# Kernel optimization log

Hardware: AMD Instinct MI355X
Metric: run time of the kernel (lower is better)

The kernel has to match this reference:

```python
import jax, jax.numpy as jnp
import numpy as np

SERIES_LEN = 4096
D_EMB = 1024
D_V = 1024
HURST = 0.7
H = HURST - 0.5          # exponent used by the module
DT = 1.0 / SERIES_LEN
EPS = 1e-8


def _attn_matrix():
    # Lower-triangular fractional power-law matrix A2[i, j]:
    #   j <  i : ((i - j) * dt + 1e-8) ** (hurst - 0.5)
    #   j == i : 1e-8 ** (hurst - 0.5)
    #   j >  i : 0
    i = jnp.arange(SERIES_LEN, dtype=jnp.int32)[:, None]
    j = jnp.arange(SERIES_LEN, dtype=jnp.int32)[None, :]
    diff = jnp.clip(i - j, 1, None).astype(jnp.float32)  # safe base for fractional power
    lower = jnp.where(i > j, (diff * DT + EPS) ** H, 0.0)
    diag = jnp.eye(SERIES_LEN, dtype=jnp.float32) * (EPS ** H)
    return lower + diag  # (L, L) float32


def setup_inputs() -> dict:
    key = jax.random.key(0)
    k1, k2 = jax.random.split(key)
    embed_series = jax.random.normal(k1, (D_EMB, SERIES_LEN), dtype=jnp.float32)
    # nn.Linear(d_emb, d_v, bias=False) weight has shape (d_v, d_emb)
    Wv_weight = jax.random.normal(k2, (D_V, D_EMB), dtype=jnp.float32) * (1.0 / np.sqrt(D_EMB))
    return {"embed_series": embed_series, "Wv_weight": Wv_weight}


def reference(embed_series, Wv_weight):
    # V (original, d_v x L) = Wv(embed_series.T).T ; output[i, c] = sum_j A2[i, j] * V[c, j]
    # => out = A2 @ (embed_series.T @ Wv_weight.T), shape (L, d_v)
    A2 = _attn_matrix()                                   # (L, L) lower triangular
    Y = jnp.einsum('el,ve->lv', embed_series, Wv_weight)  # (L, d_v)
    return A2 @ Y                                         # (L, d_v)
```

## Files before the change

kernel.cpp:

```cpp
#include <hip/hip_runtime.h>
#include <hip/hip_bf16.h>
#include <cstdint>
#include <cstddef>


#define L_SER 4096
#define DEMB  1024
#define DV    1024

#define R_STRIDE 4224
#define R_O0     4096

typedef __bf16 bf16_t;
typedef __attribute__((ext_vector_type(8))) __bf16 bf16x8;
typedef __attribute__((ext_vector_type(4))) float f32x4;

__device__ __forceinline__ void glds16(const bf16_t* g, bf16_t* l) {
    __builtin_amdgcn_global_load_lds(
        (const __attribute__((address_space(1))) unsigned int*)(const void*)g,
        (__attribute__((address_space(3))) unsigned int*)(void*)l,
        16, 0, 0);
}

__global__ void prep_kernel(const float* __restrict__ E, const float* __restrict__ W,
                            bf16_t* __restrict__ Eb, bf16_t* __restrict__ Wb,
                            bf16_t* __restrict__ R) {
    const int b = blockIdx.x;
    if (b < 132) {
        int idx = b * 256 + threadIdx.x;
        int s = idx / R_STRIDE;
        int x = idx - s * R_STRIDE;
        int d = R_O0 + s - x;
        float v = 0.0f;
        if (d >= 0 && d < L_SER)
            v = powf((d == 0) ? 1e-8f : ((float)d * (1.0f / (float)L_SER) + 1e-8f), 0.2f);
        R[idx] = (bf16_t)v;
    } else if (b < 132 + 2048) {
        int idx = (b - 132) * 256 + threadIdx.x;
        const f32x4* s = (const f32x4*)E;
        f32x4 v0 = s[idx * 2], v1 = s[idx * 2 + 1];
        bf16x8 o;
        o[0] = (bf16_t)v0[0]; o[1] = (bf16_t)v0[1]; o[2] = (bf16_t)v0[2]; o[3] = (bf16_t)v0[3];
        o[4] = (bf16_t)v1[0]; o[5] = (bf16_t)v1[1]; o[6] = (bf16_t)v1[2]; o[7] = (bf16_t)v1[3];
        ((bf16x8*)Eb)[idx] = o;
    } else {
        int idx = (b - 2180) * 256 + threadIdx.x;
        const f32x4* s = (const f32x4*)W;
        f32x4 v0 = s[idx * 2], v1 = s[idx * 2 + 1];
        bf16x8 o;
        o[0] = (bf16_t)v0[0]; o[1] = (bf16_t)v0[1]; o[2] = (bf16_t)v0[2]; o[3] = (bf16_t)v0[3];
        o[4] = (bf16_t)v1[0]; o[5] = (bf16_t)v1[1]; o[6] = (bf16_t)v1[2]; o[7] = (bf16_t)v1[3];
        ((bf16x8*)Wb)[idx] = o;
    }
}

#define GA_STAGE(SBOFS)                                                      \
    _Pragma("unroll")                                                        \
    for (int c = 0; c < 4; ++c) {                                            \
        glds16(pA[c], &sA[(SBOFS) + (c * 32 + wave * 8) * 64]);              \
        glds16(pB[c], &sB[(SBOFS) + (c * 32 + wave * 8) * 64]);              \
        pA[c] += 64; pB[c] += 64;                                            \
    }

#define GA_COMPUTE(SBOFS)                                                    \
    _Pragma("unroll")                                                        \
    for (int kk = 0; kk < 2; ++kk) {                                         \
        const int co = kk ? coff1 : coff0;                                   \
        bf16x8 afr[4], bfr[4];                                               \
        _Pragma("unroll")                                                    \
        for (int tm = 0; tm < 4; ++tm)                                       \
            afr[tm] = *(const bf16x8*)&sA[(SBOFS) + (wm * 64 + tm * 16 + ln) * 64 + co]; \
        _Pragma("unroll")                                                    \
        for (int tn = 0; tn < 4; ++tn)                                       \
            bfr[tn] = *(const bf16x8*)&sB[(SBOFS) + (wn * 64 + tn * 16 + ln) * 64 + co]; \
        _Pragma("unroll")                                                    \
        for (int tm = 0; tm < 4; ++tm)                                       \
            _Pragma("unroll")                                                \
            for (int tn = 0; tn < 4; ++tn)                                   \
                acc[tm][tn] = __builtin_amdgcn_mfma_f32_16x16x32_bf16(afr[tm], bfr[tn], acc[tm][tn], 0, 0, 0); \
    }

__global__ __launch_bounds__(256, 2) void gemm_a_kernel(const bf16_t* __restrict__ R,
                                                        const bf16_t* __restrict__ Eb,
                                                        bf16_t* __restrict__ T0,
                                                        bf16_t* __restrict__ T1) {
    __shared__ __align__(16) bf16_t sA[2 * 128 * 64];
    __shared__ __align__(16) bf16_t sB[2 * 128 * 64];

    const int bid = blockIdx.x;
    int I, nb, h;
    if (bid < 256) { I = bid >> 3;                nb = bid & 7;         h = 0; }
    else           { I = 31 - ((bid - 256) >> 3); nb = (bid - 256) & 7; h = 1; }
    const int i0 = I * 128;
    const int n0 = nb * 128;
    const int nsteps = I + 1;
    const int j0b = h ? 64 * (I + 1) : 0;
    bf16_t* __restrict__ Tout = h ? T1 : T0;

    const int tid  = threadIdx.x;
    const int wave = tid >> 6;
    const int lane = tid & 63;
    const int quad = lane >> 4;
    const int ln   = lane & 15;
    const int wm   = wave >> 1;
    const int wn   = wave & 1;

    const int lrow = lane >> 3;
    const int lch  = (lane & 7) ^ lrow;
    const int rsw   = ln & 7;
    const int coff0 = ((quad ^ rsw)) * 8;
    const int coff1 = (((4 + quad) ^ rsw)) * 8;

    f32x4 acc[4][4];
#pragma unroll
    for (int a = 0; a < 4; ++a)
#pragma unroll
        for (int b = 0; b < 4; ++b) acc[a][b] = (f32x4){0, 0, 0, 0};

    const bf16_t* pA[4];
    const bf16_t* pB[4];
#pragma unroll
    for (int c = 0; c < 4; ++c) {
        int r = c * 32 + wave * 8 + lrow;
        pA[c] = R + (size_t)(r & 7) * R_STRIDE + (R_O0 - i0 + j0b - 8 * (r >> 3) + lch * 8);
        pB[c] = Eb + (size_t)(n0 + r) * L_SER + j0b + lch * 8;
    }

    GA_STAGE(0)
    for (int s = 0;; s += 2) {
        __syncthreads();
        if (s + 1 < nsteps) { GA_STAGE(128 * 64) }
        GA_COMPUTE(0)
        if (s + 1 >= nsteps) break;
        __syncthreads();
        if (s + 2 < nsteps) { GA_STAGE(0) }
        GA_COMPUTE(128 * 64)
        if (s + 2 >= nsteps) break;
    }

#pragma unroll
    for (int tm = 0; tm < 4; ++tm) {
        int row_base = i0 + wm * 64 + tm * 16 + quad * 4;
#pragma unroll
        for (int tn = 0; tn < 4; ++tn) {
            int col = n0 + wn * 64 + tn * 16 + ln;
#pragma unroll
            for (int r = 0; r < 4; ++r)
                Tout[(size_t)(row_base + r) * DEMB + col] = (bf16_t)acc[tm][tn][r];
        }
    }
}

#define GB_STAGE_A(SBOFS, RA)                                                \
    _Pragma("unroll")                                                        \
    for (int c = 0; c < 2; ++c)                                              \
        *(bf16x8*)&sA[(SBOFS) + aofs[c]] = RA[c];

#define GB_LOAD_A(RA)                                                        \
    _Pragma("unroll")                                                        \
    for (int c = 0; c < 2; ++c) {                                            \
        bf16x8 t0 = *(const bf16x8*)p0[c];                                   \
        bf16x8 t1 = *(const bf16x8*)p1[c];                                   \
        bf16x8 o;                                                            \
        _Pragma("unroll")                                                    \
        for (int u = 0; u < 8; ++u) o[u] = (bf16_t)((float)t0[u] + (float)t1[u]); \
        RA[c] = o;                                                           \
        p0[c] += 64; p1[c] += 64;                                            \
    }

#define GB_STAGE_B(SBOFS)                                                    \
    _Pragma("unroll")                                                        \
    for (int c = 0; c < 4; ++c) {                                            \
        glds16(pW[c], &sB[(SBOFS) + (c * 32 + wave * 8) * 64]);              \
        pW[c] += 64;                                                         \
    }

#define GB_COMPUTE(SBOFS_A, SBOFS_B)                                         \
    _Pragma("unroll")                                                        \
    for (int kk = 0; kk < 2; ++kk) {                                         \
        const int co = kk ? coff1 : coff0;                                   \
        bf16x8 afr[2], bfr[4];                                               \
        _Pragma("unroll")                                                    \
        for (int tm = 0; tm < 2; ++tm)                                       \
            afr[tm] = *(const bf16x8*)&sA[(SBOFS_A) + (wm * 32 + tm * 16 + ln) * 64 + co]; \
        _Pragma("unroll")                                                    \
        for (int tn = 0; tn < 4; ++tn)                                       \
            bfr[tn] = *(const bf16x8*)&sB[(SBOFS_B) + (wn * 64 + tn * 16 + ln) * 64 + co]; \
        _Pragma("unroll")                                                    \
        for (int tm = 0; tm < 2; ++tm)                                       \
            _Pragma("unroll")                                                \
            for (int tn = 0; tn < 4; ++tn)                                   \
                acc[tm][tn] = __builtin_amdgcn_mfma_f32_16x16x32_bf16(afr[tm], bfr[tn], acc[tm][tn], 0, 0, 0); \
    }

__global__ __launch_bounds__(256, 2) void gemm_b_kernel(const bf16_t* __restrict__ T0,
                                                        const bf16_t* __restrict__ T1,
                                                        const bf16_t* __restrict__ Wb,
                                                        float* __restrict__ out) {
    __shared__ __align__(16) bf16_t sA[2 * 64 * 64];
    __shared__ __align__(16) bf16_t sB[2 * 128 * 64];

    const int bid = blockIdx.x;
    const int ib = bid >> 3;
    const int nb = bid & 7;
    const int i0 = ib * 64;
    const int n0 = nb * 128;

    const int tid  = threadIdx.x;
    const int wave = tid >> 6;
    const int lane = tid & 63;
    const int quad = lane >> 4;
    const int ln   = lane & 15;
    const int wm   = wave >> 1;
    const int wn   = wave & 1;
    const int srow = tid >> 3;
    const int t8   = tid & 7;

    const int lrow = lane >> 3;
    const int lch  = (lane & 7) ^ lrow;
    const int rsw   = ln & 7;
    const int coff0 = ((quad ^ rsw)) * 8;
    const int coff1 = (((4 + quad) ^ rsw)) * 8;

    int aofs[2];
#pragma unroll
    for (int c = 0; c < 2; ++c)
        aofs[c] = (c * 32 + srow) * 64 + (t8 ^ (srow & 7)) * 8;

    f32x4 acc[2][4];
#pragma unroll
    for (int a = 0; a < 2; ++a)
#pragma unroll
        for (int b = 0; b < 4; ++b) acc[a][b] = (f32x4){0, 0, 0, 0};

    const int nsteps = DEMB / 64;

    const bf16_t* p0[2];
    const bf16_t* p1[2];
    const bf16_t* pW[4];
    bf16x8 ra0[2], ra1[2];
#pragma unroll
    for (int c = 0; c < 2; ++c) {
        size_t arow = (size_t)(i0 + c * 32 + srow) * DEMB + t8 * 8;
        p0[c] = T0 + arow;
        p1[c] = T1 + arow;
    }
#pragma unroll
    for (int c = 0; c < 4; ++c)
        pW[c] = Wb + (size_t)(n0 + c * 32 + wave * 8 + lrow) * DEMB + lch * 8;

    GB_LOAD_A(ra0)
    GB_LOAD_A(ra1)
    GB_STAGE_B(0)

    for (int s = 0;; s += 2) {
        GB_STAGE_A(0, ra0)
        __syncthreads();
        if (s + 2 < nsteps) { GB_LOAD_A(ra0) }
        if (s + 1 < nsteps) { GB_STAGE_B(128 * 64) }
        GB_COMPUTE(0, 0)
        GB_STAGE_A(64 * 64, ra1)
        __syncthreads();
        if (s + 3 < nsteps) { GB_LOAD_A(ra1) }
        if (s + 2 < nsteps) { GB_STAGE_B(0) }
        GB_COMPUTE(64 * 64, 128 * 64)
        if (s + 2 >= nsteps) break;
    }

#pragma unroll
    for (int tm = 0; tm < 2; ++tm) {
        int row_base = i0 + wm * 32 + tm * 16 + quad * 4;
#pragma unroll
        for (int tn = 0; tn < 4; ++tn) {
            int col = n0 + wn * 64 + tn * 16 + ln;
#pragma unroll
            for (int r = 0; r < 4; ++r)
                out[(size_t)(row_base + r) * DV + col] = acc[tm][tn][r];
        }
    }
}

extern "C" void kernel_launch(void* const* d_in, const int* in_sizes, int n_in,
                              void* d_out, int out_size, void* d_ws, size_t ws_size,
                              hipStream_t stream) {
    const float* E = (const float*)d_in[0];
    const float* W = (const float*)d_in[1];
    float* out = (float*)d_out;

    char* ws = (char*)d_ws;
    bf16_t* Eb = (bf16_t*)(ws);
    bf16_t* T0 = (bf16_t*)(ws + (size_t)8  * 1024 * 1024);
    bf16_t* T1 = (bf16_t*)(ws + (size_t)16 * 1024 * 1024);
    bf16_t* Wb = (bf16_t*)(ws + (size_t)24 * 1024 * 1024);
    bf16_t* R  = (bf16_t*)(ws + (size_t)26 * 1024 * 1024);

    prep_kernel<<<2692, 256, 0, stream>>>(E, W, Eb, Wb, R);
    gemm_a_kernel<<<512, 256, 0, stream>>>(R, Eb, T0, T1);
    gemm_b_kernel<<<512, 256, 0, stream>>>(T0, T1, Wb, out);
}
```

Measured before the change: 125.0 us.

## Split long triangular rows into four K-partitions to balance gemm_a work

After: 132.9 us. +6.3%, slower.

```diff
diff --git a/kernel.cpp b/kernel.cpp
--- a/kernel.cpp
+++ b/kernel.cpp
@@ -83,19 +83,35 @@
 __global__ __launch_bounds__(256, 2) void gemm_a_kernel(const bf16_t* __restrict__ R,
                                                         const bf16_t* __restrict__ Eb,
                                                         bf16_t* __restrict__ T0,
-                                                        bf16_t* __restrict__ T1) {
+                                                        bf16_t* __restrict__ T1,
+                                                        bf16_t* __restrict__ T2,
+                                                        bf16_t* __restrict__ T3) {
     __shared__ __align__(16) bf16_t sA[2 * 128 * 64];
     __shared__ __align__(16) bf16_t sB[2 * 128 * 64];
 
     const int bid = blockIdx.x;
-    int I, nb, h;
-    if (bid < 256) { I = bid >> 3;                nb = bid & 7;         h = 0; }
-    else           { I = 31 - ((bid - 256) >> 3); nb = (bid - 256) & 7; h = 1; }
+    int I, nb, p, cs, cnt;
+    if (bid < 512) {
+        nb = bid & 7;
+        p  = (bid >> 3) & 3;
+        I  = 31 - (bid >> 5);
+        int TC = 2 * (I + 1);
+        int q = TC >> 2, rr = TC & 3;
+        cnt = q + (p < rr ? 1 : 0);
+        cs  = p * q + (p < rr ? p : rr);
+    } else {
+        int s = bid - 512;
+        nb = s & 7;
+        p  = (s >> 3) & 1;
+        I  = 15 - (s >> 4);
+        cnt = I + 1;
+        cs  = p * (I + 1);
+    }
     const int i0 = I * 128;
     const int n0 = nb * 128;
-    const int nsteps = I + 1;
-    const int j0b = h ? 64 * (I + 1) : 0;
-    bf16_t* __restrict__ Tout = h ? T1 : T0;
+    const int nsteps = cnt;
+    const int j0b = cs * 64;
+    bf16_t* __restrict__ Tout = (p == 0) ? T0 : (p == 1) ? T1 : (p == 2) ? T2 : T3;
 
     const int tid  = threadIdx.x;
     const int wave = tid >> 6;
@@ -162,8 +178,19 @@
         bf16x8 t0 = *(const bf16x8*)p0[c];                                   \
         bf16x8 t1 = *(const bf16x8*)p1[c];                                   \
         bf16x8 o;                                                            \
-        _Pragma("unroll")                                                    \
-        for (int u = 0; u < 8; ++u) o[u] = (bf16_t)((float)t0[u] + (float)t1[u]); \
+        if (fourway) {                                                       \
+            bf16x8 t2 = *(const bf16x8*)p2[c];                               \
+            bf16x8 t3 = *(const bf16x8*)p3[c];                               \
+            _Pragma("unroll")                                                \
+            for (int u = 0; u < 8; ++u)                                      \
+                o[u] = (bf16_t)(((float)t0[u] + (float)t1[u]) +              \
+                                ((float)t2[u] + (float)t3[u]));              \
+            p2[c] += 64; p3[c] += 64;                                        \
+        } else {                                                             \
+            _Pragma("unroll")                                                \
+            for (int u = 0; u < 8; ++u)                                      \
+                o[u] = (bf16_t)((float)t0[u] + (float)t1[u]);                \
+        }                                                                    \
         RA[c] = o;                                                           \
         p0[c] += 64; p1[c] += 64;                                            \
     }
@@ -195,6 +222,8 @@
 
 __global__ __launch_bounds__(256, 2) void gemm_b_kernel(const bf16_t* __restrict__ T0,
                                                         const bf16_t* __restrict__ T1,
+                                                        const bf16_t* __restrict__ T2,
+                                                        const bf16_t* __restrict__ T3,
                                                         const bf16_t* __restrict__ Wb,
                                                         float* __restrict__ out) {
     __shared__ __align__(16) bf16_t sA[2 * 64 * 64];
@@ -205,6 +234,7 @@
     const int nb = bid & 7;
     const int i0 = ib * 64;
     const int n0 = nb * 128;
+    const bool fourway = (i0 >= 2048);
 
     const int tid  = threadIdx.x;
     const int wave = tid >> 6;
@@ -237,6 +267,8 @@
 
     const bf16_t* p0[2];
     const bf16_t* p1[2];
+    const bf16_t* p2[2];
+    const bf16_t* p3[2];
     const bf16_t* pW[4];
     bf16x8 ra0[2], ra1[2];
 #pragma unroll
@@ -244,6 +276,8 @@
         size_t arow = (size_t)(i0 + c * 32 + srow) * DEMB + t8 * 8;
         p0[c] = T0 + arow;
         p1[c] = T1 + arow;
+        p2[c] = T2 + arow;
+        p3[c] = T3 + arow;
     }
 #pragma unroll
     for (int c = 0; c < 4; ++c)
@@ -291,10 +325,12 @@
     bf16_t* Eb = (bf16_t*)(ws);
     bf16_t* T0 = (bf16_t*)(ws + (size_t)8  * 1024 * 1024);
     bf16_t* T1 = (bf16_t*)(ws + (size_t)16 * 1024 * 1024);
-    bf16_t* Wb = (bf16_t*)(ws + (size_t)24 * 1024 * 1024);
-    bf16_t* R  = (bf16_t*)(ws + (size_t)26 * 1024 * 1024);
+    bf16_t* T2 = (bf16_t*)(ws + (size_t)24 * 1024 * 1024);
+    bf16_t* T3 = (bf16_t*)(ws + (size_t)32 * 1024 * 1024);
+    bf16_t* Wb = (bf16_t*)(ws + (size_t)40 * 1024 * 1024);
+    bf16_t* R  = (bf16_t*)(ws + (size_t)42 * 1024 * 1024);
 
     prep_kernel<<<2692, 256, 0, stream>>>(E, W, Eb, Wb, R);
-    gemm_a_kernel<<<512, 256, 0, stream>>>(R, Eb, T0, T1);
-    gemm_b_kernel<<<512, 256, 0, stream>>>(T0, T1, Wb, out);
-}
+    gemm_a_kernel<<<768, 256, 0, stream>>>(R, Eb, T0, T1, T2, T3);
+    gemm_b_kernel<<<512, 256, 0, stream>>>(T0, T1, T2, T3, Wb, out);
+}
```
